# Performance work log

Hardware: AMD Instinct MI355X
Metric: run time of the kernel (lower is better)

The kernel has to match this reference:

```python
import jax, jax.numpy as jnp
import numpy as np

NEG_SLOPE = 0.2  # leaky_relu_negative_slope


def setup_inputs() -> dict:
    key = jax.random.key(0)
    k = jax.random.split(key, 6)
    N = 1024          # n_nodes == nei_nodes (forced by the asserts in forward)
    IN = 256          # in_features
    OUT = 256         # out_features (nei_embedding feature dim, since linear_r = Linear(out_features, ...))
    H, F = 4, 64      # n_heads, n_hidden = out_features // n_heads
    h = jax.random.normal(k[0], (N, IN), dtype=jnp.float32)
    nei_embedding = jax.random.normal(k[1], (N, OUT), dtype=jnp.float32)
    adj_mat = jax.random.randint(k[2], (N, N), 0, 2).astype(jnp.float32)
    scale = 0.05
    w_l = jax.random.normal(k[3], (IN, H * F), dtype=jnp.float32) * scale   # linear_l.weight.T
    w_r = jax.random.normal(k[4], (OUT, H * F), dtype=jnp.float32) * scale  # linear_r.weight.T
    attn_w = jax.random.normal(k[5], (F,), dtype=jnp.float32) * scale       # attn.weight (1, F) -> (F,)
    return {"h": h, "nei_embedding": nei_embedding, "adj_mat": adj_mat,
            "w_l": w_l, "w_r": w_r, "attn_w": attn_w, "use_elu": 1}


def reference(h, nei_embedding, adj_mat, w_l, w_r, attn_w, use_elu):
    N = h.shape[0]
    M = nei_embedding.shape[0]
    F = attn_w.shape[0]
    H = w_l.shape[1] // F
    g_l = (h @ w_l).reshape(N, H, F)              # (N, H, F)
    g_r = (nei_embedding @ w_r).reshape(M, H, F)  # (M, H, F)
    # Torch does repeat/repeat_interleave then view(n, m, H, F); with the
    # assert-enforced n == m this is exactly g_sum[i, j] = g_l[j] + g_r[i].
    g_sum = g_r[:, None, :, :] + g_l[None, :, :, :]          # (N, N, H, F)
    e = jnp.einsum("nmhf,f->nmh", jax.nn.leaky_relu(g_sum, NEG_SLOPE), attn_w)
    adj_t = adj_mat.T[:, :, None]                             # (M, N, 1) -> broadcasts over heads
    e = jnp.where(adj_t == 0, -jnp.inf, e)
    exp_attention = jnp.exp(e)
    weighted = exp_attention * adj_t                          # (N, N, H)
    denom = jnp.sum(weighted, axis=1, keepdims=True)
    a = weighted / denom                                      # masked softmax over neighbors
    # dropout is identity at inference
    attn_res = jnp.einsum("ijh,jhf->ihf", a, g_r)            # (N, H, F)
    if use_elu:
        attn_res = jax.nn.elu(attn_res)
    return attn_res.reshape(N, H * F)  # is_concat=True
```

## Files before the change

kernel.cpp:

```cpp
#include <hip/hip_runtime.h>
#include <math.h>

#define NN 1024
#define KK 256
#define NH 4
#define FD 64
#define HF 256

typedef __attribute__((ext_vector_type(16))) float fx16;

#define OFF_GL   0
#define OFF_GR   (256*1024)
#define OFF_CL   (512*1024)
#define OFF_CR   (512*1024 + 4096)
#define OFF_DENP (512*1024 + 8192)
#define OFF_P    (768*1024)
#define OFF_ACCP (OFF_P + 4*1024*1024)

__global__ __launch_bounds__(256) void gatv2_gemm(
    const float* __restrict__ hmat, const float* __restrict__ nei,
    const float* __restrict__ w_l, const float* __restrict__ w_r,
    const float* __restrict__ aw, float* __restrict__ ws)
{
    __shared__ float sA[16*260];
    const int t   = threadIdx.x;
    const int mb  = blockIdx.x;
    const int hd  = blockIdx.y;
    const int mat = blockIdx.z;
    const float* A = mat ? nei : hmat;
    const float* W = mat ? w_r : w_l;
    float* G  = ws + (mat ? OFF_GR : OFF_GL);
    float* CC = ws + (mat ? OFF_CR : OFF_CL);

    #pragma unroll
    for (int rep = 0; rep < 4; ++rep) {
        const int flat = rep*256 + t;
        const int r = flat >> 6, c = (flat & 63) << 2;
        *(float4*)&sA[r*260 + c] = *(const float4*)&A[(size_t)(mb*16 + r)*KK + c];
    }
    __syncthreads();

    const int m  = t >> 4;
    const int nq = t & 15;
    const int ng = hd*64 + (nq << 2);
    const float* Wp = W + ng;

    float4 acc = make_float4(0.f, 0.f, 0.f, 0.f);
    #pragma unroll 4
    for (int k0 = 0; k0 < KK; k0 += 4) {
        const float4 a4 = *(const float4*)&sA[m*260 + k0];
        const float4 w0 = *(const float4*)(Wp + (size_t)(k0+0)*HF);
        const float4 w1 = *(const float4*)(Wp + (size_t)(k0+1)*HF);
        const float4 w2 = *(const float4*)(Wp + (size_t)(k0+2)*HF);
        const float4 w3 = *(const float4*)(Wp + (size_t)(k0+3)*HF);
        acc.x += a4.x*w0.x; acc.y += a4.x*w0.y; acc.z += a4.x*w0.z; acc.w += a4.x*w0.w;
        acc.x += a4.y*w1.x; acc.y += a4.y*w1.y; acc.z += a4.y*w1.z; acc.w += a4.y*w1.w;
        acc.x += a4.z*w2.x; acc.y += a4.z*w2.y; acc.z += a4.z*w2.z; acc.w += a4.z*w2.w;
        acc.x += a4.w*w3.x; acc.y += a4.w*w3.y; acc.z += a4.w*w3.z; acc.w += a4.w*w3.w;
    }

    *(float4*)&G[(size_t)(mb*16 + m)*HF + ng] = acc;

    {
        const float4 w4 = ((const float4*)aw)[nq];
        float wd = w4.x*acc.x + w4.y*acc.y + w4.z*acc.z + w4.w*acc.w;
        wd += __shfl_xor(wd, 1);
        wd += __shfl_xor(wd, 2);
        wd += __shfl_xor(wd, 4);
        wd += __shfl_xor(wd, 8);
        if (nq == 0) CC[hd*NN + mb*16 + m] = 0.6f*wd;
    }
}

#define EBLK(RV, QB)                                                \
    { _Pragma("unroll") for (int q = 0; q < 4; ++q) {               \
        const float4 wq = w[(QB)+q]; const float4 gq = gri[(QB)+q]; \
        e0 += wq.x * fabsf(RV[q*4+0] + gq.x);                       \
        e1 += wq.y * fabsf(RV[q*4+1] + gq.y);                       \
        e2 += wq.z * fabsf(RV[q*4+2] + gq.z);                       \
        e3 += wq.w * fabsf(RV[q*4+3] + gq.w); } }

__global__ __launch_bounds__(256, 3) void gatv2_e(
    const float* __restrict__ wsro, const float* __restrict__ adj,
    const float* __restrict__ aw, float* __restrict__ P,
    float* __restrict__ denP)
{
    __shared__ float s_w[64];
    const float* g_l = wsro + OFF_GL;
    const float* g_r = wsro + OFF_GR;
    const float* cl  = wsro + OFF_CL;
    const float* cr  = wsro + OFF_CR;
    const int t  = threadIdx.x;
    const int jc = blockIdx.x;
    const int ib = blockIdx.y;
    const int hh = blockIdx.z;
    const int i  = ib*256 + t;

    if (t < 16) ((float4*)s_w)[t] = ((const float4*)aw)[t];
    __syncthreads();

    float4 w[16], gri[16];
    {
        const float4* gp = (const float4*)(g_r + (size_t)i*HF + hh*FD);
        #pragma unroll
        for (int q = 0; q < 16; ++q) {
            w[q]   = ((const float4*)s_w)[q];
            gri[q] = gp[q];
        }
    }
    const float cri = cr[hh*NN + i];

    float denl = 0.f;
    const int j0 = jc*32;
    for (int jj = 0; jj < 32; ++jj) {
        const int j = j0 + jj;
        const float mask = adj[(size_t)j*NN + i];
        fx16 r0, r1, r2, r3; float clv;
        const float* rowp = g_l + (size_t)j*HF + hh*FD;
        const float* clp  = cl + hh*NN + j;
        asm volatile(
            "s_load_dwordx16 %0, %5, 0x0\n\t"
            "s_load_dwordx16 %1, %5, 0x40\n\t"
            "s_load_dwordx16 %2, %5, 0x80\n\t"
            "s_load_dwordx16 %3, %5, 0xc0\n\t"
            "s_load_dword %4, %6, 0x0\n\t"
            "s_waitcnt lgkmcnt(0)"
            : "=s"(r0), "=s"(r1), "=s"(r2), "=s"(r3), "=s"(clv)
            : "s"(rowp), "s"(clp));
        float e0 = 0.f, e1 = 0.f, e2 = 0.f, e3 = 0.f;
        EBLK(r0, 0) EBLK(r1, 4) EBLK(r2, 8) EBLK(r3, 12)
        const float e  = cri + clv + 0.4f*((e0+e1)+(e2+e3));
        const float pw = (mask != 0.f) ? __expf(e) : 0.f;
        denl += pw;
        P[((size_t)hh*NN + j)*NN + i] = pw;
    }
    denP[(size_t)jc*(NN*NH) + hh*NN + i] = denl;
}

#define PVFMA(G0, G1, PP)                                           \
    { _Pragma("unroll") for (int q = 0; q < 4; ++q) {               \
        acc[q].x   += (PP)*G0[q*4+0]; acc[q].y   += (PP)*G0[q*4+1]; \
        acc[q].z   += (PP)*G0[q*4+2]; acc[q].w   += (PP)*G0[q*4+3]; \
        acc[4+q].x += (PP)*G1[q*4+0]; acc[4+q].y += (PP)*G1[q*4+1]; \
        acc[4+q].z += (PP)*G1[q*4+2]; acc[4+q].w += (PP)*G1[q*4+3]; } }

__global__ __launch_bounds__(256, 4) void gatv2_pv(
    const float* __restrict__ wsro, float* __restrict__ accP)
{
    __shared__ float sT[256*36];
    const float* g_r = wsro + OFF_GR;
    const float* P   = wsro + OFF_P;
    const int t  = threadIdx.x;
    const int jc = blockIdx.x;
    const int ib = blockIdx.y;
    const int fs = blockIdx.z;
    const int hh = fs >> 1;
    const int f0 = hh*64 + (fs & 1)*32;
    const int i  = ib*256 + t;

    float4 acc[8];
    #pragma unroll
    for (int q = 0; q < 8; ++q) acc[q] = make_float4(0.f,0.f,0.f,0.f);

    const int j0 = jc*32;
    const size_t pb0 = ((size_t)hh*NN)*NN + i;

    fx16 a0, a1, b0, b1;
    {
        const float* gp = g_r + (size_t)j0*HF + f0;
        asm volatile(
            "s_load_dwordx16 %0, %2, 0x0\n\t"
            "s_load_dwordx16 %1, %2, 0x40\n\t"
            "s_waitcnt lgkmcnt(0)"
            : "=s"(a0), "=s"(a1) : "s"(gp));
    }
    float pA = P[pb0 + (size_t)j0*NN];

    for (int jj = 0; jj < 32; jj += 2) {
        const int j = j0 + jj;
        {
            const float* gp = g_r + (size_t)(j+1)*HF + f0;
            asm volatile(
                "s_load_dwordx16 %0, %2, 0x0\n\t"
                "s_load_dwordx16 %1, %2, 0x40"
                : "=s"(b0), "=s"(b1) : "s"(gp));
        }
        const float pB = P[pb0 + (size_t)(j+1)*NN];
        PVFMA(a0, a1, pA)
        asm volatile("s_waitcnt lgkmcnt(0)");
        {
            const int j2 = (jj + 2 < 32) ? (j + 2) : j0;
            const float* gp = g_r + (size_t)j2*HF + f0;
            asm volatile(
                "s_load_dwordx16 %0, %2, 0x0\n\t"
                "s_load_dwordx16 %1, %2, 0x40"
                : "=s"(a0), "=s"(a1) : "s"(gp));
            pA = P[pb0 + (size_t)j2*NN];
        }
        PVFMA(b0, b1, pB)
        asm volatile("s_waitcnt lgkmcnt(0)");
    }

    #pragma unroll
    for (int q = 0; q < 8; ++q)
        *(float4*)&sT[t*36 + q*4] = acc[q];
    __syncthreads();
    #pragma unroll
    for (int rep = 0; rep < 8; ++rep) {
        const int idx = rep*256 + t;
        const int il = idx >> 3, fq = idx & 7;
        const float4 v = *(const float4*)&sT[il*36 + fq*4];
        *(float4*)&accP[(size_t)jc*(NN*HF) + (size_t)(ib*256 + il)*HF + f0 + fq*4] = v;
    }
}

__global__ __launch_bounds__(256) void gatv2_fin(
    const float* __restrict__ accP, const float* __restrict__ denP,
    const int* __restrict__ use_elu, float* __restrict__ out)
{
    const int idx4 = blockIdx.x*256 + threadIdx.x;
    const int i  = idx4 >> 6;
    const int hh = (idx4 >> 4) & 3;
    float4 s = make_float4(0.f,0.f,0.f,0.f);
    for (int c = 0; c < 32; ++c) {
        const float4 v = *(const float4*)&accP[(size_t)c*(NN*HF) + (size_t)idx4*4];
        s.x += v.x; s.y += v.y; s.z += v.z; s.w += v.w;
    }
    float d = 0.f;
    for (int c = 0; c < 32; ++c) d += denP[(size_t)c*(NN*NH) + hh*NN + i];
    const float rd = 1.f / d;
    float4 r = make_float4(s.x*rd, s.y*rd, s.z*rd, s.w*rd);
    if (*use_elu != 0) {
        r.x = (r.x > 0.f) ? r.x : expm1f(r.x);
        r.y = (r.y > 0.f) ? r.y : expm1f(r.y);
        r.z = (r.z > 0.f) ? r.z : expm1f(r.z);
        r.w = (r.w > 0.f) ? r.w : expm1f(r.w);
    }
    ((float4*)out)[idx4] = r;
}

extern "C" void kernel_launch(void* const* d_in, const int* in_sizes, int n_in,
                              void* d_out, int out_size, void* d_ws, size_t ws_size,
                              hipStream_t stream)
{
    const float* hmat = (const float*)d_in[0];
    const float* nei  = (const float*)d_in[1];
    const float* adj  = (const float*)d_in[2];
    const float* w_l  = (const float*)d_in[3];
    const float* w_r  = (const float*)d_in[4];
    const float* aw   = (const float*)d_in[5];
    const int*   uel  = (const int*)d_in[6];
    float* out = (float*)d_out;
    float* ws  = (float*)d_ws;

    hipLaunchKernelGGL(gatv2_gemm, dim3(64,4,2), dim3(256), 0, stream,
                       hmat, nei, w_l, w_r, aw, ws);
    hipLaunchKernelGGL(gatv2_e, dim3(32,4,4), dim3(256), 0, stream,
                       ws, adj, aw, ws + OFF_P, ws + OFF_DENP);
    hipLaunchKernelGGL(gatv2_pv, dim3(32,4,8), dim3(256), 0, stream,
                       ws, ws + OFF_ACCP);
    hipLaunchKernelGGL(gatv2_fin, dim3((NN*HF)/1024), dim3(256), 0, stream,
                       ws + OFF_ACCP, ws + OFF_DENP, uel, out);
}
```

Measured before the change: 140.0 us.

## Fuse attention score and PV accumulation kernels, eliminating the P matrix round trip

Merges the score/exp kernel and the P·g_r accumulation kernel into one kernel that accumulates the weighted g_r row per neighbor directly in registers. This removes writing and re-reading the full N×N×H probability matrix and one kernel launch. It also prefetches the adjacency mask one iteration ahead. The cost is 64 extra accumulator registers per thread, lower occupancy, and an uncoalesced per-thread partial output layout.

```diff
diff --git a/kernel.cpp b/kernel.cpp
--- a/kernel.cpp
+++ b/kernel.cpp
@@ -14,8 +14,7 @@
 #define OFF_CL   (512*1024)
 #define OFF_CR   (512*1024 + 4096)
 #define OFF_DENP (512*1024 + 8192)
-#define OFF_P    (768*1024)
-#define OFF_ACCP (OFF_P + 4*1024*1024)
+#define OFF_ACCP (768*1024)
 
 __global__ __launch_bounds__(256) void gatv2_gemm(
     const float* __restrict__ hmat, const float* __restrict__ nei,
@@ -80,10 +79,17 @@
         e2 += wq.z * fabsf(RV[q*4+2] + gq.z);                       \
         e3 += wq.w * fabsf(RV[q*4+3] + gq.w); } }
 
-__global__ __launch_bounds__(256, 3) void gatv2_e(
+#define PVACC(RV, QB)                                               \
+    { _Pragma("unroll") for (int q = 0; q < 4; ++q) {               \
+        acc[(QB)+q].x += pw*RV[q*4+0];                              \
+        acc[(QB)+q].y += pw*RV[q*4+1];                              \
+        acc[(QB)+q].z += pw*RV[q*4+2];                              \
+        acc[(QB)+q].w += pw*RV[q*4+3]; } }
+
+__global__ __launch_bounds__(256, 2) void gatv2_attn(
     const float* __restrict__ wsro, const float* __restrict__ adj,
-    const float* __restrict__ aw, float* __restrict__ P,
-    float* __restrict__ denP)
+    const float* __restrict__ aw,
+    float* __restrict__ accP, float* __restrict__ denP)
 {
     __shared__ float s_w[64];
     const float* g_l = wsro + OFF_GL;
@@ -110,108 +116,56 @@
     }
     const float cri = cr[hh*NN + i];
 
+    float4 acc[16];
+    #pragma unroll
+    for (int q = 0; q < 16; ++q) acc[q] = make_float4(0.f,0.f,0.f,0.f);
     float denl = 0.f;
+
     const int j0 = jc*32;
+    float mask_next = adj[(size_t)j0*NN + i];
     for (int jj = 0; jj < 32; ++jj) {
         const int j = j0 + jj;
-        const float mask = adj[(size_t)j*NN + i];
+        const float mask = mask_next;
+        if (jj + 1 < 32) mask_next = adj[(size_t)(j + 1)*NN + i];
+
         fx16 r0, r1, r2, r3; float clv;
-        const float* rowp = g_l + (size_t)j*HF + hh*FD;
-        const float* clp  = cl + hh*NN + j;
-        asm volatile(
-            "s_load_dwordx16 %0, %5, 0x0\n\t"
-            "s_load_dwordx16 %1, %5, 0x40\n\t"
-            "s_load_dwordx16 %2, %5, 0x80\n\t"
-            "s_load_dwordx16 %3, %5, 0xc0\n\t"
-            "s_load_dword %4, %6, 0x0\n\t"
-            "s_waitcnt lgkmcnt(0)"
-            : "=s"(r0), "=s"(r1), "=s"(r2), "=s"(r3), "=s"(clv)
-            : "s"(rowp), "s"(clp));
+        {
+            const float* rowp = g_l + (size_t)j*HF + hh*FD;
+            const float* clp  = cl + hh*NN + j;
+            asm volatile(
+                "s_load_dwordx16 %0, %5, 0x0\n\t"
+                "s_load_dwordx16 %1, %5, 0x40\n\t"
+                "s_load_dwordx16 %2, %5, 0x80\n\t"
+                "s_load_dwordx16 %3, %5, 0xc0\n\t"
+                "s_load_dword %4, %6, 0x0\n\t"
+                "s_waitcnt lgkmcnt(0)"
+                : "=s"(r0), "=s"(r1), "=s"(r2), "=s"(r3), "=s"(clv)
+                : "s"(rowp), "s"(clp));
+        }
         float e0 = 0.f, e1 = 0.f, e2 = 0.f, e3 = 0.f;
         EBLK(r0, 0) EBLK(r1, 4) EBLK(r2, 8) EBLK(r3, 12)
         const float e  = cri + clv + 0.4f*((e0+e1)+(e2+e3));
         const float pw = (mask != 0.f) ? __expf(e) : 0.f;
         denl += pw;
-        P[((size_t)hh*NN + j)*NN + i] = pw;
-    }
+
+        {
+            const float* rowp = g_r + (size_t)j*HF + hh*FD;
+            asm volatile(
+                "s_load_dwordx16 %0, %4, 0x0\n\t"
+                "s_load_dwordx16 %1, %4, 0x40\n\t"
+                "s_load_dwordx16 %2, %4, 0x80\n\t"
+                "s_load_dwordx16 %3, %4, 0xc0\n\t"
+                "s_waitcnt lgkmcnt(0)"
+                : "=s"(r0), "=s"(r1), "=s"(r2), "=s"(r3)
+                : "s"(rowp));
+        }
+        PVACC(r0, 0) PVACC(r1, 4) PVACC(r2, 8) PVACC(r3, 12)
+    }
+
+    float* op = accP + (size_t)jc*(NN*HF) + ((size_t)i*NH + hh)*FD;
+    #pragma unroll
+    for (int q = 0; q < 16; ++q) ((float4*)op)[q] = acc[q];
     denP[(size_t)jc*(NN*NH) + hh*NN + i] = denl;
-}
-
-#define PVFMA(G0, G1, PP)                                           \
-    { _Pragma("unroll") for (int q = 0; q < 4; ++q) {               \
-        acc[q].x   += (PP)*G0[q*4+0]; acc[q].y   += (PP)*G0[q*4+1]; \
-        acc[q].z   += (PP)*G0[q*4+2]; acc[q].w   += (PP)*G0[q*4+3]; \
-        acc[4+q].x += (PP)*G1[q*4+0]; acc[4+q].y += (PP)*G1[q*4+1]; \
-        acc[4+q].z += (PP)*G1[q*4+2]; acc[4+q].w += (PP)*G1[q*4+3]; } }
-
-__global__ __launch_bounds__(256, 4) void gatv2_pv(
-    const float* __restrict__ wsro, float* __restrict__ accP)
-{
-    __shared__ float sT[256*36];
-    const float* g_r = wsro + OFF_GR;
-    const float* P   = wsro + OFF_P;
-    const int t  = threadIdx.x;
-    const int jc = blockIdx.x;
-    const int ib = blockIdx.y;
-    const int fs = blockIdx.z;
-    const int hh = fs >> 1;
-    const int f0 = hh*64 + (fs & 1)*32;
-    const int i  = ib*256 + t;
-
-    float4 acc[8];
-    #pragma unroll
-    for (int q = 0; q < 8; ++q) acc[q] = make_float4(0.f,0.f,0.f,0.f);
-
-    const int j0 = jc*32;
-    const size_t pb0 = ((size_t)hh*NN)*NN + i;
-
-    fx16 a0, a1, b0, b1;
-    {
-        const float* gp = g_r + (size_t)j0*HF + f0;
-        asm volatile(
-            "s_load_dwordx16 %0, %2, 0x0\n\t"
-            "s_load_dwordx16 %1, %2, 0x40\n\t"
-            "s_waitcnt lgkmcnt(0)"
-            : "=s"(a0), "=s"(a1) : "s"(gp));
-    }
-    float pA = P[pb0 + (size_t)j0*NN];
-
-    for (int jj = 0; jj < 32; jj += 2) {
-        const int j = j0 + jj;
-        {
-            const float* gp = g_r + (size_t)(j+1)*HF + f0;
-            asm volatile(
-                "s_load_dwordx16 %0, %2, 0x0\n\t"
-                "s_load_dwordx16 %1, %2, 0x40"
-                : "=s"(b0), "=s"(b1) : "s"(gp));
-        }
-        const float pB = P[pb0 + (size_t)(j+1)*NN];
-        PVFMA(a0, a1, pA)
-        asm volatile("s_waitcnt lgkmcnt(0)");
-        {
-            const int j2 = (jj + 2 < 32) ? (j + 2) : j0;
-            const float* gp = g_r + (size_t)j2*HF + f0;
-            asm volatile(
-                "s_load_dwordx16 %0, %2, 0x0\n\t"
-                "s_load_dwordx16 %1, %2, 0x40"
-                : "=s"(a0), "=s"(a1) : "s"(gp));
-            pA = P[pb0 + (size_t)j2*NN];
-        }
-        PVFMA(b0, b1, pB)
-        asm volatile("s_waitcnt lgkmcnt(0)");
-    }
-
-    #pragma unroll
-    for (int q = 0; q < 8; ++q)
-        *(float4*)&sT[t*36 + q*4] = acc[q];
-    __syncthreads();
-    #pragma unroll
-    for (int rep = 0; rep < 8; ++rep) {
-        const int idx = rep*256 + t;
-        const int il = idx >> 3, fq = idx & 7;
-        const float4 v = *(const float4*)&sT[il*36 + fq*4];
-        *(float4*)&accP[(size_t)jc*(NN*HF) + (size_t)(ib*256 + il)*HF + f0 + fq*4] = v;
-    }
 }
 
 __global__ __launch_bounds__(256) void gatv2_fin(
@@ -255,10 +209,8 @@
 
     hipLaunchKernelGGL(gatv2_gemm, dim3(64,4,2), dim3(256), 0, stream,
                        hmat, nei, w_l, w_r, aw, ws);
-    hipLaunchKernelGGL(gatv2_e, dim3(32,4,4), dim3(256), 0, stream,
-                       ws, adj, aw, ws + OFF_P, ws + OFF_DENP);
-    hipLaunchKernelGGL(gatv2_pv, dim3(32,4,8), dim3(256), 0, stream,
-                       ws, ws + OFF_ACCP);
+    hipLaunchKernelGGL(gatv2_attn, dim3(32,4,4), dim3(256), 0, stream,
+                       ws, adj, aw, ws + OFF_ACCP, ws + OFF_DENP);
     hipLaunchKernelGGL(gatv2_fin, dim3((NN*HF)/1024), dim3(256), 0, stream,
                        ws + OFF_ACCP, ws + OFF_DENP, uel, out);
 }
```

Result: no change. 141.5 us (+1.1%).

## Presort and prescale attention features by weight sign to drop per-element multiplies

Applied to the files above, without the earlier changes.

A new prep kernel reorders the 64 feature lanes by the sign of attn_w and stores |w|, so the GEMM writes |w|-scaled, sign-grouped copies of g_l and g_r (padded to 68). The score kernel then needs only adds and abs per lane, with one ±0.4 factor per group of four, which removes the per-element weight multiply. The score kernel also moves from scalar loads of g_l to an LDS tile, and each thread now computes two i rows over 16 j instead of one row over 32 j, so the denominator partials double to 64. The cost is extra workspace, a memset, a tiny extra launch, and higher register pressure (occupancy hint lowered to 2).

```diff
diff --git a/kernel.cpp b/kernel.cpp
--- a/kernel.cpp
+++ b/kernel.cpp
@@ -6,16 +6,40 @@
 #define NH 4
 #define FD 64
 #define HF 256
+#define RL 68
+#define NG 17
 
 typedef __attribute__((ext_vector_type(16))) float fx16;
-
-#define OFF_GL   0
-#define OFF_GR   (256*1024)
-#define OFF_CL   (512*1024)
-#define OFF_CR   (512*1024 + 4096)
-#define OFF_DENP (512*1024 + 8192)
-#define OFF_P    (768*1024)
-#define OFF_ACCP (OFF_P + 4*1024*1024)
+typedef __attribute__((ext_vector_type(4)))  float fx4;
+
+#define OFF_GR    0
+#define OFF_GL2   262144
+#define OFF_GR2   540672
+#define OFF_CL    819200
+#define OFF_CR    823296
+#define OFF_DENP  827392
+#define OFF_P     1089536
+#define OFF_ACCP  5283840
+#define OFF_DEST  13672448
+#define OFF_ABSW  13672512
+#define OFF_GPOS  13672576
+
+__global__ void gatv2_prep(const float* __restrict__ aw, float* __restrict__ ws)
+{
+    const int f = threadIdx.x;
+    const float wv = aw[f];
+    const bool pos = (wv >= 0.f);
+    const unsigned long long mask = __ballot(pos);
+    const int npos  = __popcll(mask);
+    const int npos4 = (npos + 3) & ~3;
+    const unsigned long long lt = (1ull << f) - 1ull;
+    const int prank = __popcll(mask & lt);
+    const int nrank = __popcll(~mask & lt);
+    const int dest  = pos ? prank : (npos4 + nrank);
+    ((int*)(ws + OFF_DEST))[f] = dest;
+    (ws + OFF_ABSW)[f] = fabsf(wv);
+    if (f == 0) ((int*)(ws + OFF_GPOS))[0] = npos4 >> 2;
+}
 
 __global__ __launch_bounds__(256) void gatv2_gemm(
     const float* __restrict__ hmat, const float* __restrict__ nei,
@@ -29,7 +53,6 @@
     const int mat = blockIdx.z;
     const float* A = mat ? nei : hmat;
     const float* W = mat ? w_r : w_l;
-    float* G  = ws + (mat ? OFF_GR : OFF_GL);
     float* CC = ws + (mat ? OFF_CR : OFF_CL);
 
     #pragma unroll
@@ -59,7 +82,17 @@
         acc.x += a4.w*w3.x; acc.y += a4.w*w3.y; acc.z += a4.w*w3.z; acc.w += a4.w*w3.w;
     }
 
-    *(float4*)&G[(size_t)(mb*16 + m)*HF + ng] = acc;
+    const int node = mb*16 + m;
+    if (mat) *(float4*)&(ws + OFF_GR)[(size_t)node*HF + ng] = acc;
+
+    {
+        const int*   destp = (const int*)(ws + OFF_DEST);
+        const int4   dv = ((const int4*)destp)[nq];
+        const float4 av = ((const float4*)(ws + OFF_ABSW))[nq];
+        float* g2 = ws + (mat ? OFF_GR2 : OFF_GL2) + ((size_t)node*NH + hd)*RL;
+        g2[dv.x] = av.x*acc.x; g2[dv.y] = av.y*acc.y;
+        g2[dv.z] = av.z*acc.z; g2[dv.w] = av.w*acc.w;
+    }
 
     {
         const float4 w4 = ((const float4*)aw)[nq];
@@ -68,73 +101,86 @@
         wd += __shfl_xor(wd, 2);
         wd += __shfl_xor(wd, 4);
         wd += __shfl_xor(wd, 8);
-        if (nq == 0) CC[hd*NN + mb*16 + m] = 0.6f*wd;
-    }
-}
-
-#define EBLK(RV, QB)                                                \
-    { _Pragma("unroll") for (int q = 0; q < 4; ++q) {               \
-        const float4 wq = w[(QB)+q]; const float4 gq = gri[(QB)+q]; \
-        e0 += wq.x * fabsf(RV[q*4+0] + gq.x);                       \
-        e1 += wq.y * fabsf(RV[q*4+1] + gq.y);                       \
-        e2 += wq.z * fabsf(RV[q*4+2] + gq.z);                       \
-        e3 += wq.w * fabsf(RV[q*4+3] + gq.w); } }
-
-__global__ __launch_bounds__(256, 3) void gatv2_e(
+        if (nq == 0) CC[hd*NN + node] = 0.6f*wd;
+    }
+}
+
+__global__ __launch_bounds__(256, 2) void gatv2_e(
     const float* __restrict__ wsro, const float* __restrict__ adj,
-    const float* __restrict__ aw, float* __restrict__ P,
-    float* __restrict__ denP)
-{
-    __shared__ float s_w[64];
-    const float* g_l = wsro + OFF_GL;
-    const float* g_r = wsro + OFF_GR;
+    float* __restrict__ P, float* __restrict__ denP)
+{
+    __shared__ float sgl[16*RL];
+    __shared__ float scl[16];
+    const float* gl2 = wsro + OFF_GL2;
+    const float* gr2 = wsro + OFF_GR2;
     const float* cl  = wsro + OFF_CL;
     const float* cr  = wsro + OFF_CR;
     const int t  = threadIdx.x;
     const int jc = blockIdx.x;
     const int ib = blockIdx.y;
     const int hh = blockIdx.z;
-    const int i  = ib*256 + t;
-
-    if (t < 16) ((float4*)s_w)[t] = ((const float4*)aw)[t];
+    const int i0 = ib*512 + t;
+    const int i1 = i0 + 256;
+    const int j0 = jc*16;
+
+    for (int idx = t; idx < 16*NG; idx += 256) {
+        const int r = idx / NG, c = idx - r*NG;
+        *(float4*)&sgl[r*RL + (c<<2)] =
+            *(const float4*)&gl2[((size_t)(j0+r)*NH + hh)*RL + (c<<2)];
+    }
+    if (t < 16) scl[t] = cl[hh*NN + j0 + t];
+
+    fx4 ga[NG], gb[NG];
+    {
+        const fx4* pa = (const fx4*)(gr2 + ((size_t)i0*NH + hh)*RL);
+        const fx4* pb = (const fx4*)(gr2 + ((size_t)i1*NH + hh)*RL);
+        #pragma unroll
+        for (int g = 0; g < NG; ++g) { ga[g] = pa[g]; gb[g] = pb[g]; }
+    }
+    #pragma unroll
+    for (int g = 0; g < NG; ++g) { asm volatile("" : "+v"(ga[g])); }
+    #pragma unroll
+    for (int g = 0; g < NG; ++g) { asm volatile("" : "+v"(gb[g])); }
+
+    const int gpos = ((const int*)(wsro + OFF_GPOS))[0];
+    float mg[NG];
+    #pragma unroll
+    for (int g = 0; g < NG; ++g) mg[g] = (g < gpos) ? 0.4f : -0.4f;
+    #pragma unroll
+    for (int g = 0; g < NG; ++g) { asm volatile("" : "+v"(mg[g])); }
+
+    const float cr0 = cr[hh*NN + i0];
+    const float cr1 = cr[hh*NN + i1];
+
+    float den0 = 0.f, den1 = 0.f;
     __syncthreads();
 
-    float4 w[16], gri[16];
-    {
-        const float4* gp = (const float4*)(g_r + (size_t)i*HF + hh*FD);
+    #pragma unroll 2
+    for (int jj = 0; jj < 16; ++jj) {
+        const int j = j0 + jj;
+        const float mk0 = adj[(size_t)j*NN + i0];
+        const float mk1 = adj[(size_t)j*NN + i1];
+        float a0 = 0.f, a1 = 0.f;
         #pragma unroll
-        for (int q = 0; q < 16; ++q) {
-            w[q]   = ((const float4*)s_w)[q];
-            gri[q] = gp[q];
+        for (int g = 0; g < NG; ++g) {
+            const fx4 b  = *(const fx4*)&sgl[jj*RL + (g<<2)];
+            const fx4 va = b + ga[g];
+            const fx4 vb = b + gb[g];
+            const float sa = (fabsf(va[0]) + fabsf(va[1])) + (fabsf(va[2]) + fabsf(va[3]));
+            const float sb = (fabsf(vb[0]) + fabsf(vb[1])) + (fabsf(vb[2]) + fabsf(vb[3]));
+            a0 = fmaf(mg[g], sa, a0);
+            a1 = fmaf(mg[g], sb, a1);
         }
-    }
-    const float cri = cr[hh*NN + i];
-
-    float denl = 0.f;
-    const int j0 = jc*32;
-    for (int jj = 0; jj < 32; ++jj) {
-        const int j = j0 + jj;
-        const float mask = adj[(size_t)j*NN + i];
-        fx16 r0, r1, r2, r3; float clv;
-        const float* rowp = g_l + (size_t)j*HF + hh*FD;
-        const float* clp  = cl + hh*NN + j;
-        asm volatile(
-            "s_load_dwordx16 %0, %5, 0x0\n\t"
-            "s_load_dwordx16 %1, %5, 0x40\n\t"
-            "s_load_dwordx16 %2, %5, 0x80\n\t"
-            "s_load_dwordx16 %3, %5, 0xc0\n\t"
-            "s_load_dword %4, %6, 0x0\n\t"
-            "s_waitcnt lgkmcnt(0)"
-            : "=s"(r0), "=s"(r1), "=s"(r2), "=s"(r3), "=s"(clv)
-            : "s"(rowp), "s"(clp));
-        float e0 = 0.f, e1 = 0.f, e2 = 0.f, e3 = 0.f;
-        EBLK(r0, 0) EBLK(r1, 4) EBLK(r2, 8) EBLK(r3, 12)
-        const float e  = cri + clv + 0.4f*((e0+e1)+(e2+e3));
-        const float pw = (mask != 0.f) ? __expf(e) : 0.f;
-        denl += pw;
-        P[((size_t)hh*NN + j)*NN + i] = pw;
-    }
-    denP[(size_t)jc*(NN*NH) + hh*NN + i] = denl;
+        const float clj = scl[jj];
+        const float p0 = (mk0 != 0.f) ? __expf(cr0 + clj + a0) : 0.f;
+        const float p1 = (mk1 != 0.f) ? __expf(cr1 + clj + a1) : 0.f;
+        den0 += p0; den1 += p1;
+        const size_t pb = ((size_t)hh*NN + j)*NN;
+        P[pb + i0] = p0;
+        P[pb + i1] = p1;
+    }
+    denP[((size_t)jc*NH + hh)*NN + i0] = den0;
+    denP[((size_t)jc*NH + hh)*NN + i1] = den1;
 }
 
 #define PVFMA(G0, G1, PP)                                           \
@@ -202,8 +248,10 @@
     }
 
     #pragma unroll
-    for (int q = 0; q < 8; ++q)
+    for (int q = 0; q < 4; ++q) {
         *(float4*)&sT[t*36 + q*4] = acc[q];
+        *(float4*)&sT[t*36 + 16 + q*4] = acc[4+q];
+    }
     __syncthreads();
     #pragma unroll
     for (int rep = 0; rep < 8; ++rep) {
@@ -227,7 +275,7 @@
         s.x += v.x; s.y += v.y; s.z += v.z; s.w += v.w;
     }
     float d = 0.f;
-    for (int c = 0; c < 32; ++c) d += denP[(size_t)c*(NN*NH) + hh*NN + i];
+    for (int c = 0; c < 64; ++c) d += denP[((size_t)c*NH + hh)*NN + i];
     const float rd = 1.f / d;
     float4 r = make_float4(s.x*rd, s.y*rd, s.z*rd, s.w*rd);
     if (*use_elu != 0) {
@@ -253,10 +301,12 @@
     float* out = (float*)d_out;
     float* ws  = (float*)d_ws;
 
+    hipMemsetAsync((void*)(ws + OFF_GL2), 0, (size_t)2*278528*sizeof(float), stream);
+    hipLaunchKernelGGL(gatv2_prep, dim3(1), dim3(64), 0, stream, aw, ws);
     hipLaunchKernelGGL(gatv2_gemm, dim3(64,4,2), dim3(256), 0, stream,
                        hmat, nei, w_l, w_r, aw, ws);
-    hipLaunchKernelGGL(gatv2_e, dim3(32,4,4), dim3(256), 0, stream,
-                       ws, adj, aw, ws + OFF_P, ws + OFF_DENP);
+    hipLaunchKernelGGL(gatv2_e, dim3(64,2,4), dim3(256), 0, stream,
+                       ws, adj, ws + OFF_P, ws + OFF_DENP);
     hipLaunchKernelGGL(gatv2_pv, dim3(32,4,8), dim3(256), 0, stream,
                        ws, ws + OFF_ACCP);
     hipLaunchKernelGGL(gatv2_fin, dim3((NN*HF)/1024), dim3(256), 0, stream,
```

After: 147.2 us. 1.05x slower.
